# Kernel optimization log

Hardware: AMD Instinct MI355X
Metric: run time of the kernel (lower is better)

Reference implementation:

```python
import jax, jax.numpy as jnp
from jax import lax
import numpy as np

B, S, E, H, T = 32, 512, 300, 512, 9


def setup_inputs() -> dict:
    key = jax.random.key(0)
    ks = jax.random.split(key, 20)
    sc = 0.1
    inp = {
        'word_embedding': jax.random.normal(ks[0], (B, S, E), jnp.float32),
        'target_tag': jax.random.randint(ks[1], (B, S), 0, T, jnp.int64),
        'attention_masks': jnp.ones((B, S), jnp.int32),
        # layer 0 LSTM params, stacked over 2 directions; PyTorch gate order i,f,g,o
        'w_ih_l0': jax.random.normal(ks[2], (2, 4 * H, E), jnp.float32) * sc,
        'w_hh_l0': jax.random.normal(ks[3], (2, 4 * H, H), jnp.float32) * sc,
        'b_ih_l0': jax.random.normal(ks[4], (2, 4 * H), jnp.float32) * sc,
        'b_hh_l0': jax.random.normal(ks[5], (2, 4 * H), jnp.float32) * sc,
        # layer 1 takes the concatenated bidirectional output (2H)
        'w_ih_l1': jax.random.normal(ks[6], (2, 4 * H, 2 * H), jnp.float32) * sc,
        'w_hh_l1': jax.random.normal(ks[7], (2, 4 * H, H), jnp.float32) * sc,
        'b_ih_l1': jax.random.normal(ks[8], (2, 4 * H), jnp.float32) * sc,
        'b_hh_l1': jax.random.normal(ks[9], (2, 4 * H), jnp.float32) * sc,
        # hidden2tag linear
        'proj_w': jax.random.normal(ks[10], (T, 2 * H), jnp.float32) * sc,
        'proj_b': jax.random.normal(ks[11], (T,), jnp.float32) * sc,
        # CRF params
        'transitions': jax.random.normal(ks[12], (T, T), jnp.float32) * sc,
        'start_trans': jax.random.normal(ks[13], (T,), jnp.float32) * sc,
        'end_trans': jax.random.normal(ks[14], (T,), jnp.float32) * sc,
    }
    return inp


def _lstm_dir(x, w_ih, w_hh, b_ih, b_hh, reverse):
    # x: [B,S,D]; precompute input contribution for all steps, scan over time.
    h0 = jnp.zeros((x.shape[0], w_hh.shape[1]), x.dtype)
    xg = jnp.einsum('bsd,gd->sbg', x, w_ih) + b_ih  # [S,B,4H]
    if reverse:
        xg = xg[::-1]

    def step(carry, g):
        h, c = carry
        g = g + h @ w_hh.T + b_hh
        i, f, gg, o = jnp.split(g, 4, axis=-1)
        c = jax.nn.sigmoid(f) * c + jax.nn.sigmoid(i) * jnp.tanh(gg)
        h = jax.nn.sigmoid(o) * jnp.tanh(c)
        return (h, c), h

    _, hs = lax.scan(step, (h0, h0), xg)  # [S,B,H]
    if reverse:
        hs = hs[::-1]
    return jnp.swapaxes(hs, 0, 1)  # [B,S,H]


def _bilstm_layer(x, w_ih, w_hh, b_ih, b_hh):
    fwd = _lstm_dir(x, w_ih[0], w_hh[0], b_ih[0], b_hh[0], False)
    bwd = _lstm_dir(x, w_ih[1], w_hh[1], b_ih[1], b_hh[1], True)
    return jnp.concatenate([fwd, bwd], axis=-1)  # [B,S,2H]


def _crf_nll(emissions, tags, mask, trans, start, end):
    # emissions: [B,S,T]; tags: [B,S] int; mask: [B,S] bool-like (first step on)
    maskf = mask.astype(emissions.dtype)
    tags = tags.astype(jnp.int32)
    # numerator: score of the gold path
    emit_sc = jnp.take_along_axis(emissions, tags[..., None], axis=-1)[..., 0]  # [B,S]
    trans_sc = trans[tags[:, :-1], tags[:, 1:]]  # [B,S-1]
    num = start[tags[:, 0]] + emit_sc[:, 0]
    num = num + jnp.sum((emit_sc[:, 1:] + trans_sc) * maskf[:, 1:], axis=1)
    last_idx = jnp.sum(mask.astype(jnp.int32), axis=1) - 1  # [B]
    last_tag = jnp.take_along_axis(tags, last_idx[:, None], axis=1)[:, 0]
    num = num + end[last_tag]
    # denominator: forward algorithm (DP scan over time)
    alpha0 = start[None, :] + emissions[:, 0]  # [B,T]

    def step(alpha, xs):
        emit_t, m_t = xs  # [B,T], [B]
        nxt = jax.scipy.special.logsumexp(alpha[:, :, None] + trans[None], axis=1) + emit_t
        return jnp.where(m_t[:, None], nxt, alpha), None

    em_t = jnp.swapaxes(emissions, 0, 1)[1:]            # [S-1,B,T]
    m_t = jnp.swapaxes(mask, 0, 1)[1:].astype(bool)     # [S-1,B]
    alpha, _ = lax.scan(step, alpha0, (em_t, m_t))
    denom = jax.scipy.special.logsumexp(alpha + end[None, :], axis=1)  # [B]
    return -jnp.mean(num - denom)


def reference(word_embedding, target_tag, attention_masks,
              w_ih_l0, w_hh_l0, b_ih_l0, b_hh_l0,
              w_ih_l1, w_hh_l1, b_ih_l1, b_hh_l1,
              proj_w, proj_b, transitions, start_trans, end_trans):
    h = _bilstm_layer(word_embedding, w_ih_l0, w_hh_l0, b_ih_l0, b_hh_l0)
    h = _bilstm_layer(h, w_ih_l1, w_hh_l1, b_ih_l1, b_hh_l1)
    # dropout is identity in eval-mode reference
    emissions = jnp.einsum('bsh,th->bst', h, proj_w) + proj_b  # [B,S,T]
    return _crf_nll(emissions, target_tag, attention_masks,
                    transitions, start_trans, end_trans)
```

## Files before the change

### kernel.cpp

```cpp
#include <hip/hip_runtime.h>
#include <hip/hip_bf16.h>
#include <math.h>

#define S_LEN 512
#define BATCH 32
#define HDIM  512
#define NTAG  9
#define M_ROWS (S_LEN * BATCH)
#define GATES  4096

typedef __hip_bfloat16 bf16;
typedef unsigned long long ull;
typedef float f32x4 __attribute__((ext_vector_type(4)));
typedef float f32x16 __attribute__((ext_vector_type(16)));
typedef short bfrag8 __attribute__((ext_vector_type(8)));

__device__ __forceinline__ float bf2f(short s) {
    unsigned u = ((unsigned)(unsigned short)s) << 16;
    return __builtin_bit_cast(float, u);
}
__device__ __forceinline__ short f2bf(float f) {
    __hip_bfloat16 h = __float2bfloat16(f);
    return __builtin_bit_cast(short, h);
}
__device__ __forceinline__ float fsig(float x) {
    return __builtin_amdgcn_rcpf(1.f + __expf(-x));
}
__device__ __forceinline__ float ftanh(float x) {
    return 1.f - 2.f * __builtin_amdgcn_rcpf(1.f + __expf(2.f * x));
}

template <int AMODE>
__global__ __launch_bounds__(256) void gemm_xg(const void* __restrict__ Ap,
                                               const float* __restrict__ Bw,
                                               int K, int KT,
                                               const float* __restrict__ bias1,
                                               const float* __restrict__ bias2,
                                               short* __restrict__ xg) {
    __shared__ char smem[32768];
    char* As = smem;
    char* Bs = smem + 16384;
    const int tid = threadIdx.x;
    const int bm = blockIdx.y * 128;
    const int bn = blockIdx.x * 128;
    const int l  = tid & 63;
    const int wv = tid >> 6;
    const int wr = wv >> 1, wc = wv & 1;

    f32x4 acc[4][4] = {};

    const int r_st  = tid >> 1;
    const int kh    = tid & 1;
    const int xorr  = (r_st & 7) << 4;

    for (int kt = 0; kt < KT; kt++) {
        const int k0 = kt * 64;
        if (AMODE == 0) {
            const float* A = (const float*)Ap;
            int mg = bm + r_st;
            const float* arow = A + ((size_t)(mg & 31) * S_LEN + (mg >> 5)) * 300;
#pragma unroll
            for (int u = 0; u < 8; u++) {
                int kk = k0 + kh * 32 + u * 4;
                float4 v = make_float4(0.f, 0.f, 0.f, 0.f);
                if (kk + 4 <= K) v = *(const float4*)(arow + kk);
                short4 sv = make_short4(f2bf(v.x), f2bf(v.y), f2bf(v.z), f2bf(v.w));
                *(short4*)(As + ((r_st * 128 + (kh * 64 + u * 8)) ^ xorr)) = sv;
            }
        } else {
            const short* A = (const short*)Ap;
            const short* arow = A + (size_t)(bm + r_st) * 1024;
#pragma unroll
            for (int u = 0; u < 4; u++) {
                int kk = k0 + kh * 32 + u * 8;
                bfrag8 v = *(const bfrag8*)(arow + kk);
                *(bfrag8*)(As + ((r_st * 128 + (kh * 64 + u * 16)) ^ xorr)) = v;
            }
        }
        {
            const float* brow = Bw + (size_t)(bn + r_st) * K;
#pragma unroll
            for (int u = 0; u < 8; u++) {
                int kk = k0 + kh * 32 + u * 4;
                float4 v = make_float4(0.f, 0.f, 0.f, 0.f);
                if (kk + 4 <= K) v = *(const float4*)(brow + kk);
                short4 sv = make_short4(f2bf(v.x), f2bf(v.y), f2bf(v.z), f2bf(v.w));
                *(short4*)(Bs + ((r_st * 128 + (kh * 64 + u * 8)) ^ xorr)) = sv;
            }
        }
        __syncthreads();
#pragma unroll
        for (int kf = 0; kf < 2; kf++) {
            bfrag8 af[4], bfr[4];
#pragma unroll
            for (int ms = 0; ms < 4; ms++) {
                int row = wr * 64 + ms * 16 + (l & 15);
                af[ms] = *(const bfrag8*)(As + ((row * 128 + kf * 64 + (l >> 4) * 16) ^ ((row & 7) << 4)));
            }
#pragma unroll
            for (int ns = 0; ns < 4; ns++) {
                int row = wc * 64 + ns * 16 + (l & 15);
                bfr[ns] = *(const bfrag8*)(Bs + ((row * 128 + kf * 64 + (l >> 4) * 16) ^ ((row & 7) << 4)));
            }
#pragma unroll
            for (int ms = 0; ms < 4; ms++)
#pragma unroll
                for (int ns = 0; ns < 4; ns++)
                    acc[ms][ns] = __builtin_amdgcn_mfma_f32_16x16x32_bf16(af[ms], bfr[ns], acc[ms][ns], 0, 0, 0);
        }
        __syncthreads();
    }
#pragma unroll
    for (int ns = 0; ns < 4; ns++) {
        int n = bn + wc * 64 + ns * 16 + (l & 15);
        float bsum = bias1[n] + bias2[n];
#pragma unroll
        for (int ms = 0; ms < 4; ms++) {
#pragma unroll
            for (int r = 0; r < 4; r++) {
                int m = bm + wr * 64 + ms * 16 + (l >> 4) * 4 + r;
                xg[(size_t)m * GATES + n] = f2bf(acc[ms][ns][r] + bsum);
            }
        }
    }
}

__global__ __launch_bounds__(512, 1) void lstm_scan(const short* __restrict__ xg,
                                                    const float* __restrict__ whh,
                                                    ull* __restrict__ pub,
                                                    short* __restrict__ hseq) {
    const int wg  = blockIdx.x;
    const int dir = wg >> 3;
    const int p   = wg & 7;
    const int tid = threadIdx.x;
    const int wv  = tid >> 6;
    const int l   = tid & 63;
    const int g   = wv >> 1;
    const int jb  = (wv & 1) * 32;
    const int qh  = l >> 5;
    const int col = l & 31;

    __shared__ char hst[32768];
    __shared__ float Cb[4][32][64];

    bfrag8 wf[32];
    {
        const int n_row = g * 512 + p * 64 + jb + col;
        const float* sp = whh + ((size_t)dir * 2048 + n_row) * 512;
#pragma unroll
        for (int ks = 0; ks < 32; ks++) {
            const float* q = sp + ks * 16 + qh * 8;
            bfrag8 v;
#pragma unroll
            for (int u = 0; u < 8; u++) v[u] = f2bf(q[u]);
            wf[ks] = v;
        }
    }

    const int bg = tid >> 4;
    const int jq = tid & 15;
    float c4[4] = {0.f, 0.f, 0.f, 0.f};

    short4 xr_cur[4], xr_nxt[4];
    {
        const int s0 = dir ? (S_LEN - 1) : 0;
        size_t xoff = ((size_t)s0 * BATCH + bg) * GATES + dir * 2048 + p * 64 + jq * 4;
#pragma unroll
        for (int g2 = 0; g2 < 4; g2++) xr_cur[g2] = *(const short4*)(xg + xoff + g2 * 512);
    }

    for (int t = 0; t < S_LEN; t++) {
        const int s = dir ? (S_LEN - 1 - t) : t;
        {
            const int tn = (t + 1 < S_LEN) ? t + 1 : t;
            const int sn = dir ? (S_LEN - 1 - tn) : tn;
            size_t xoff = ((size_t)sn * BATCH + bg) * GATES + dir * 2048 + p * 64 + jq * 4;
#pragma unroll
            for (int g2 = 0; g2 < 4; g2++) xr_nxt[g2] = *(const short4*)(xg + xoff + g2 * 512);
        }
        const ull* src = pub + (size_t)((t & 1) * 2 + dir) * 8192;
        const unsigned expect = (unsigned)t;
        ull wvv[16];
        {
            int rounds = 0;
            bool ok;
            do {
                if (rounds++) __builtin_amdgcn_s_sleep(1);
                ok = true;
#pragma unroll
                for (int i = 0; i < 16; i++) {
                    wvv[i] = __hip_atomic_load(src + tid + i * 512, __ATOMIC_RELAXED,
                                               __HIP_MEMORY_SCOPE_AGENT);
                    ok &= ((unsigned)(wvv[i] >> 32) == expect);
                }
                if (rounds > (1 << 14)) break;
            } while (!__all(ok));
        }
#pragma unroll
        for (int i = 0; i < 16; i++) {
            int w = tid + i * 512;
            int b = w >> 8, kp = w & 255;
            *(unsigned*)(hst + ((b * 1024 + kp * 4) ^ ((b & 15) << 4))) = (unsigned)wvv[i];
        }
        __syncthreads();
        f32x16 acc = {};
#pragma unroll
        for (int ks = 0; ks < 32; ks++) {
            int byte = col * 1024 + ks * 32 + qh * 16;
            const bfrag8 a = *(const bfrag8*)(hst + (byte ^ ((col & 15) << 4)));
            acc = __builtin_amdgcn_mfma_f32_32x32x16_bf16(a, wf[ks], acc, 0, 0, 0);
        }
#pragma unroll
        for (int r = 0; r < 16; r++) {
            int brow = (r & 3) + 8 * (r >> 2) + 4 * qh;
            Cb[g][brow][jb + col] = acc[r];
        }
        __syncthreads();
        float hv[4];
        {
            float xi[4] = {bf2f(xr_cur[0].x), bf2f(xr_cur[0].y), bf2f(xr_cur[0].z), bf2f(xr_cur[0].w)};
            float xf[4] = {bf2f(xr_cur[1].x), bf2f(xr_cur[1].y), bf2f(xr_cur[1].z), bf2f(xr_cur[1].w)};
            float xc[4] = {bf2f(xr_cur[2].x), bf2f(xr_cur[2].y), bf2f(xr_cur[2].z), bf2f(xr_cur[2].w)};
            float xo[4] = {bf2f(xr_cur[3].x), bf2f(xr_cur[3].y), bf2f(xr_cur[3].z), bf2f(xr_cur[3].w)};
#pragma unroll
            for (int q = 0; q < 4; q++) {
                int jl = jq * 4 + q;
                float gi = Cb[0][bg][jl] + xi[q];
                float gf = Cb[1][bg][jl] + xf[q];
                float gc = Cb[2][bg][jl] + xc[q];
                float go = Cb[3][bg][jl] + xo[q];
                float cc = fsig(gf) * c4[q] + fsig(gi) * ftanh(gc);
                c4[q] = cc;
                hv[q] = fsig(go) * ftanh(cc);
            }
        }
        {
            unsigned short h0 = (unsigned short)f2bf(hv[0]);
            unsigned short h1 = (unsigned short)f2bf(hv[1]);
            unsigned short h2 = (unsigned short)f2bf(hv[2]);
            unsigned short h3 = (unsigned short)f2bf(hv[3]);
            ull tagw = (ull)(unsigned)(t + 1) << 32;
            ull w0 = tagw | (ull)h0 | ((ull)h1 << 16);
            ull w1 = tagw | (ull)h2 | ((ull)h3 << 16);
            ull* dst = pub + (size_t)(((t + 1) & 1) * 2 + dir) * 8192 + bg * 256 + p * 32 + jq * 2;
            __hip_atomic_store(dst, w0, __ATOMIC_RELAXED, __HIP_MEMORY_SCOPE_AGENT);
            __hip_atomic_store(dst + 1, w1, __ATOMIC_RELAXED, __HIP_MEMORY_SCOPE_AGENT);
            ull pk = (ull)h0 | ((ull)h1 << 16) | ((ull)h2 << 32) | ((ull)h3 << 48);
            ull* hd = (ull*)(hseq + ((size_t)s * BATCH + bg) * 1024 + dir * HDIM + p * 64 + jq * 4);
            __builtin_nontemporal_store(pk, hd);
        }
#pragma unroll
        for (int g2 = 0; g2 < 4; g2++) xr_cur[g2] = xr_nxt[g2];
    }
}

__global__ __launch_bounds__(256) void proj_kernel(const bf16* __restrict__ h1,
                                                   const float* __restrict__ pw,
                                                   const float* __restrict__ pb,
                                                   float* __restrict__ em) {
    __shared__ float wl[NTAG * 1024];
    __shared__ float bl[NTAG];
    for (int i = threadIdx.x; i < NTAG * 1024; i += 256) wl[i] = pw[i];
    if (threadIdx.x < NTAG) bl[threadIdx.x] = pb[threadIdx.x];
    __syncthreads();
    int m = blockIdx.x * 256 + threadIdx.x;
    int s = m >> 5, b = m & 31;
    const bf16* hr = h1 + (size_t)m * 1024;
    float acc[NTAG] = {};
    for (int k = 0; k < 1024; k += 8) {
        uint4 raw = *(const uint4*)(hr + k);
        const bf16* hv = (const bf16*)&raw;
        float hf[8];
#pragma unroll
        for (int u = 0; u < 8; u++) hf[u] = __bfloat162float(hv[u]);
#pragma unroll
        for (int tt = 0; tt < NTAG; tt++) {
            const float* wrow = &wl[tt * 1024 + k];
#pragma unroll
            for (int u = 0; u < 8; u++) acc[tt] += hf[u] * wrow[u];
        }
    }
#pragma unroll
    for (int tt = 0; tt < NTAG; tt++)
        em[((size_t)b * S_LEN + s) * NTAG + tt] = acc[tt] + bl[tt];
}

__global__ __launch_bounds__(64) void crf_kernel(const float* __restrict__ em,
                                                 const int* __restrict__ tags,
                                                 const int* __restrict__ mask,
                                                 const float* __restrict__ trans,
                                                 const float* __restrict__ startv,
                                                 const float* __restrict__ endv,
                                                 float* __restrict__ out_b) {
    int b = blockIdx.x;
    int lane = threadIdx.x;
    const float* E = em + (size_t)b * S_LEN * NTAG;
    const int* tg = tags + (size_t)b * S_LEN;
    const int* mk = mask + (size_t)b * S_LEN;

    float np = 0.f;
    int msum = 0;
    for (int s = lane; s < S_LEN; s += 64) {
        msum += (mk[s] != 0);
        if (s >= 1) {
            float mf = (float)mk[s];
            int ts = tg[s], tp = tg[s - 1];
            np += (E[(size_t)s * NTAG + ts] + trans[tp * NTAG + ts]) * mf;
        }
    }
    for (int off = 32; off; off >>= 1) {
        np += __shfl_down(np, off);
        msum += __shfl_down(msum, off);
    }
    np = __shfl(np, 0);
    msum = __shfl(msum, 0);

    int j = lane;
    float tcol[NTAG];
    if (j < NTAG)
#pragma unroll
        for (int i = 0; i < NTAG; i++) tcol[i] = trans[i * NTAG + j];
    float alpha = (j < NTAG) ? (startv[j] + E[j]) : -1e30f;
    for (int s = 1; s < S_LEN; s++) {
        float av[NTAG];
#pragma unroll
        for (int i = 0; i < NTAG; i++) av[i] = __shfl(alpha, i);
        if (j < NTAG) {
            float m = -1e30f;
#pragma unroll
            for (int i = 0; i < NTAG; i++) m = fmaxf(m, av[i] + tcol[i]);
            float ss = 0.f;
#pragma unroll
            for (int i = 0; i < NTAG; i++) ss += __expf(av[i] + tcol[i] - m);
            float nxt = m + __logf(ss) + E[(size_t)s * NTAG + j];
            if (mk[s] != 0) alpha = nxt;
        }
    }
    float val = (j < NTAG) ? (alpha + endv[j]) : -1e30f;
    float m2 = -1e30f, vv;
#pragma unroll
    for (int i = 0; i < NTAG; i++) { vv = __shfl(val, i); m2 = fmaxf(m2, vv); }
    float s2 = 0.f;
#pragma unroll
    for (int i = 0; i < NTAG; i++) { vv = __shfl(val, i); s2 += __expf(vv - m2); }
    float denom = m2 + __logf(s2);
    if (lane == 0) {
        int t0 = tg[0];
        int last = msum - 1;
        if (last < 0) last = 0;
        int lt = tg[last];
        float num = startv[t0] + E[t0] + np + endv[lt];
        out_b[b] = num - denom;
    }
}

__global__ __launch_bounds__(64) void finalize(const float* __restrict__ out_b,
                                               float* __restrict__ out) {
    int lane = threadIdx.x;
    float v = (lane < BATCH) ? out_b[lane] : 0.f;
    for (int off = 32; off; off >>= 1) v += __shfl_down(v, off);
    if (lane == 0) out[0] = -v / (float)BATCH;
}

extern "C" void kernel_launch(void* const* d_in, const int* in_sizes, int n_in,
                              void* d_out, int out_size, void* d_ws, size_t ws_size,
                              hipStream_t stream) {
    const float* x      = (const float*)d_in[0];
    const int*   tags   = (const int*)d_in[1];
    const int*   mask   = (const int*)d_in[2];
    const float* w_ih0  = (const float*)d_in[3];
    const float* w_hh0  = (const float*)d_in[4];
    const float* b_ih0  = (const float*)d_in[5];
    const float* b_hh0  = (const float*)d_in[6];
    const float* w_ih1  = (const float*)d_in[7];
    const float* w_hh1  = (const float*)d_in[8];
    const float* b_ih1  = (const float*)d_in[9];
    const float* b_hh1  = (const float*)d_in[10];
    const float* pw     = (const float*)d_in[11];
    const float* pb     = (const float*)d_in[12];
    const float* trans  = (const float*)d_in[13];
    const float* startv = (const float*)d_in[14];
    const float* endv   = (const float*)d_in[15];

    char* ws = (char*)d_ws;
    size_t off = 0;
    short* xg    = (short*)(ws + off); off += (size_t)M_ROWS * GATES * 2;
    short* hseq  = (short*)(ws + off); off += (size_t)M_ROWS * 1024 * 2;
    ull*   pub   = (ull*)(ws + off);   off += (size_t)2 * 2 * 8192 * 8;
    float* emis  = (float*)(ws + off); off += (size_t)BATCH * S_LEN * NTAG * 4;
    float* outb  = (float*)(ws + off); off += 256;
    if (off > ws_size) return;

    const size_t pub_bytes = (size_t)2 * 2 * 8192 * 8;

    gemm_xg<0><<<dim3(32, 128), 256, 0, stream>>>(x, w_ih0, 300, 5, b_ih0, b_hh0, xg);
    hipMemsetAsync(pub, 0, pub_bytes, stream);
    lstm_scan<<<16, 512, 0, stream>>>(xg, w_hh0, pub, hseq);

    gemm_xg<1><<<dim3(32, 128), 256, 0, stream>>>(hseq, w_ih1, 1024, 16, b_ih1, b_hh1, xg);
    hipMemsetAsync(pub, 0, pub_bytes, stream);
    lstm_scan<<<16, 512, 0, stream>>>(xg, w_hh1, pub, hseq);

    proj_kernel<<<M_ROWS / 256, 256, 0, stream>>>((const bf16*)hseq, pw, pb, emis);
    crf_kernel<<<BATCH, 64, 0, stream>>>(emis, tags, mask, trans, startv, endv, outb);
    finalize<<<1, 64, 0, stream>>>(outb, (float*)d_out);
}
```

Before: 6.590 ms.

## Split recurrent matmul over K halves per wave, reusing each A fragment twice

Each wave in the LSTM scan now covers one gate and half of the K dimension across both 32-column halves, instead of one gate/column half over the full K. Each LDS A-fragment load now feeds two independent MFMA chains, which halves LDS reads of h per wave and gives two interleaved accumulators for better MFMA latency hiding. The cost is a split-K partial-sum reduction through a doubled, padded Cb shared buffer, plus extra LDS traffic in the gate epilogue.

```diff
diff --git a/kernel.cpp b/kernel.cpp
--- a/kernel.cpp
+++ b/kernel.cpp
@@ -135,25 +135,26 @@
     const int tid = threadIdx.x;
     const int wv  = tid >> 6;
     const int l   = tid & 63;
-    const int g   = wv >> 1;
-    const int jb  = (wv & 1) * 32;
+    const int g   = wv & 3;
+    const int kh2 = wv >> 2;
     const int qh  = l >> 5;
     const int col = l & 31;
 
     __shared__ char hst[32768];
-    __shared__ float Cb[4][32][64];
-
-    bfrag8 wf[32];
-    {
-        const int n_row = g * 512 + p * 64 + jb + col;
-        const float* sp = whh + ((size_t)dir * 2048 + n_row) * 512;
-#pragma unroll
-        for (int ks = 0; ks < 32; ks++) {
+    __shared__ float Cb[2][4][32][65];
+
+    bfrag8 wf[2][16];
+#pragma unroll
+    for (int jj2 = 0; jj2 < 2; jj2++) {
+        const float* sp = whh + ((size_t)dir * 2048 + g * 512 + p * 64 + jj2 * 32 + col) * 512
+                        + kh2 * 256;
+#pragma unroll
+        for (int ks = 0; ks < 16; ks++) {
             const float* q = sp + ks * 16 + qh * 8;
             bfrag8 v;
 #pragma unroll
             for (int u = 0; u < 8; u++) v[u] = f2bf(q[u]);
-            wf[ks] = v;
+            wf[jj2][ks] = v;
         }
     }
 
@@ -203,17 +204,19 @@
             *(unsigned*)(hst + ((b * 1024 + kp * 4) ^ ((b & 15) << 4))) = (unsigned)wvv[i];
         }
         __syncthreads();
-        f32x16 acc = {};
-#pragma unroll
-        for (int ks = 0; ks < 32; ks++) {
-            int byte = col * 1024 + ks * 32 + qh * 16;
+        f32x16 acc0 = {}, acc1 = {};
+#pragma unroll
+        for (int ks = 0; ks < 16; ks++) {
+            int byte = col * 1024 + kh2 * 512 + ks * 32 + qh * 16;
             const bfrag8 a = *(const bfrag8*)(hst + (byte ^ ((col & 15) << 4)));
-            acc = __builtin_amdgcn_mfma_f32_32x32x16_bf16(a, wf[ks], acc, 0, 0, 0);
+            acc0 = __builtin_amdgcn_mfma_f32_32x32x16_bf16(a, wf[0][ks], acc0, 0, 0, 0);
+            acc1 = __builtin_amdgcn_mfma_f32_32x32x16_bf16(a, wf[1][ks], acc1, 0, 0, 0);
         }
 #pragma unroll
         for (int r = 0; r < 16; r++) {
             int brow = (r & 3) + 8 * (r >> 2) + 4 * qh;
-            Cb[g][brow][jb + col] = acc[r];
+            Cb[kh2][g][brow][col]      = acc0[r];
+            Cb[kh2][g][brow][32 + col] = acc1[r];
         }
         __syncthreads();
         float hv[4];
@@ -225,10 +228,10 @@
 #pragma unroll
             for (int q = 0; q < 4; q++) {
                 int jl = jq * 4 + q;
-                float gi = Cb[0][bg][jl] + xi[q];
-                float gf = Cb[1][bg][jl] + xf[q];
-                float gc = Cb[2][bg][jl] + xc[q];
-                float go = Cb[3][bg][jl] + xo[q];
+                float gi = Cb[0][0][bg][jl] + Cb[1][0][bg][jl] + xi[q];
+                float gf = Cb[0][1][bg][jl] + Cb[1][1][bg][jl] + xf[q];
+                float gc = Cb[0][2][bg][jl] + Cb[1][2][bg][jl] + xc[q];
+                float go = Cb[0][3][bg][jl] + Cb[1][3][bg][jl] + xo[q];
                 float cc = fsig(gf) * c4[q] + fsig(gi) * ftanh(gc);
                 c4[q] = cc;
                 hv[q] = fsig(go) * ftanh(cc);
```

Result: no change. 6.712 ms (+1.9%).

## Co-locate each LSTM direction's workgroups on one XCC for faster handoff

Applied to the files above, without the earlier changes.

The recurrent scan kernel now launches 256 workgroups. Each reads its hardware XCC ID and claims one of 8 roles per XCC through an atomic ticket, so both directions' 8 cooperating workgroups run on XCC 0 and XCC 1 and the rest exit right away. Keeping each direction's communicating workgroups on one XCC is meant to keep the per-step hidden-state exchange inside that XCC's shared L2 rather than crossing the die. Polling now uses volatile loads and stores, falling back to atomic loads after many rounds. A per-layer tag base plus each block seeding its own slot replaces the memset of the exchange buffer. The scheme relies on the dispatcher placing at least 8 resident blocks on each of those XCCs, and on volatile accesses giving enough visibility, otherwise the spin loop can stall until its bailout.

```diff
diff --git a/kernel.cpp b/kernel.cpp
--- a/kernel.cpp
+++ b/kernel.cpp
@@ -127,12 +127,31 @@
 
 __global__ __launch_bounds__(512, 1) void lstm_scan(const short* __restrict__ xg,
                                                     const float* __restrict__ whh,
-                                                    ull* __restrict__ pub,
-                                                    short* __restrict__ hseq) {
-    const int wg  = blockIdx.x;
-    const int dir = wg >> 3;
-    const int p   = wg & 7;
+                                                    ull* pub,
+                                                    short* __restrict__ hseq,
+                                                    int* tick,
+                                                    int tagbase) {
     const int tid = threadIdx.x;
+
+    __shared__ int role_sh;
+    if (tid == 0) {
+        unsigned xcc;
+        asm volatile("s_getreg_b32 %0, hwreg(HW_REG_XCC_ID)" : "=s"(xcc));
+        xcc &= 7;
+        int r = -1;
+        if (xcc < 2) {
+            int tk = __hip_atomic_fetch_add(&tick[xcc], 1, __ATOMIC_RELAXED,
+                                            __HIP_MEMORY_SCOPE_AGENT);
+            if (tk < 8) r = (int)xcc * 8 + tk;
+        }
+        role_sh = r;
+    }
+    __syncthreads();
+    const int role = role_sh;
+    if (role < 0) return;
+
+    const int dir = role >> 3;
+    const int p   = role & 7;
     const int wv  = tid >> 6;
     const int l   = tid & 63;
     const int g   = wv >> 1;
@@ -143,6 +162,16 @@
     __shared__ char hst[32768];
     __shared__ float Cb[4][32][64];
 
+    const int bg = tid >> 4;
+    const int jq = tid & 15;
+
+    {
+        ull tagw = (ull)(unsigned)tagbase << 32;
+        volatile ull* dst = pub + (size_t)(0 * 2 + dir) * 8192 + bg * 256 + p * 32 + jq * 2;
+        dst[0] = tagw;
+        dst[1] = tagw;
+    }
+
     bfrag8 wf[32];
     {
         const int n_row = g * 512 + p * 64 + jb + col;
@@ -157,8 +186,6 @@
         }
     }
 
-    const int bg = tid >> 4;
-    const int jq = tid & 15;
     float c4[4] = {0.f, 0.f, 0.f, 0.f};
 
     short4 xr_cur[4], xr_nxt[4];
@@ -179,22 +206,28 @@
             for (int g2 = 0; g2 < 4; g2++) xr_nxt[g2] = *(const short4*)(xg + xoff + g2 * 512);
         }
         const ull* src = pub + (size_t)((t & 1) * 2 + dir) * 8192;
-        const unsigned expect = (unsigned)t;
+        const volatile ull* srcv = (const volatile ull*)src;
+        const unsigned expect = (unsigned)(tagbase + t);
         ull wvv[16];
         {
             int rounds = 0;
-            bool ok;
-            do {
-                if (rounds++) __builtin_amdgcn_s_sleep(1);
-                ok = true;
-#pragma unroll
-                for (int i = 0; i < 16; i++) {
-                    wvv[i] = __hip_atomic_load(src + tid + i * 512, __ATOMIC_RELAXED,
-                                               __HIP_MEMORY_SCOPE_AGENT);
-                    ok &= ((unsigned)(wvv[i] >> 32) == expect);
+            for (;;) {
+                bool ok = true;
+                if (rounds < 1024) {
+#pragma unroll
+                    for (int i = 0; i < 16; i++) wvv[i] = srcv[tid + i * 512];
+                } else {
+#pragma unroll
+                    for (int i = 0; i < 16; i++)
+                        wvv[i] = __hip_atomic_load(src + tid + i * 512, __ATOMIC_RELAXED,
+                                                   __HIP_MEMORY_SCOPE_AGENT);
                 }
-                if (rounds > (1 << 14)) break;
-            } while (!__all(ok));
+#pragma unroll
+                for (int i = 0; i < 16; i++) ok &= ((unsigned)(wvv[i] >> 32) == expect);
+                if (__all(ok)) break;
+                if (++rounds > (1 << 15)) break;
+                __builtin_amdgcn_s_sleep(1);
+            }
         }
 #pragma unroll
         for (int i = 0; i < 16; i++) {
@@ -239,12 +272,12 @@
             unsigned short h1 = (unsigned short)f2bf(hv[1]);
             unsigned short h2 = (unsigned short)f2bf(hv[2]);
             unsigned short h3 = (unsigned short)f2bf(hv[3]);
-            ull tagw = (ull)(unsigned)(t + 1) << 32;
+            ull tagw = (ull)(unsigned)(tagbase + t + 1) << 32;
             ull w0 = tagw | (ull)h0 | ((ull)h1 << 16);
             ull w1 = tagw | (ull)h2 | ((ull)h3 << 16);
-            ull* dst = pub + (size_t)(((t + 1) & 1) * 2 + dir) * 8192 + bg * 256 + p * 32 + jq * 2;
-            __hip_atomic_store(dst, w0, __ATOMIC_RELAXED, __HIP_MEMORY_SCOPE_AGENT);
-            __hip_atomic_store(dst + 1, w1, __ATOMIC_RELAXED, __HIP_MEMORY_SCOPE_AGENT);
+            volatile ull* dst = pub + (size_t)(((t + 1) & 1) * 2 + dir) * 8192 + bg * 256 + p * 32 + jq * 2;
+            dst[0] = w0;
+            dst[1] = w1;
             ull pk = (ull)h0 | ((ull)h1 << 16) | ((ull)h2 << 32) | ((ull)h3 << 48);
             ull* hd = (ull*)(hseq + ((size_t)s * BATCH + bg) * 1024 + dir * HDIM + p * 64 + jq * 4);
             __builtin_nontemporal_store(pk, hd);
@@ -387,19 +420,18 @@
     short* xg    = (short*)(ws + off); off += (size_t)M_ROWS * GATES * 2;
     short* hseq  = (short*)(ws + off); off += (size_t)M_ROWS * 1024 * 2;
     ull*   pub   = (ull*)(ws + off);   off += (size_t)2 * 2 * 8192 * 8;
+    int*   tick  = (int*)(ws + off);   off += 256;
     float* emis  = (float*)(ws + off); off += (size_t)BATCH * S_LEN * NTAG * 4;
     float* outb  = (float*)(ws + off); off += 256;
     if (off > ws_size) return;
 
-    const size_t pub_bytes = (size_t)2 * 2 * 8192 * 8;
-
     gemm_xg<0><<<dim3(32, 128), 256, 0, stream>>>(x, w_ih0, 300, 5, b_ih0, b_hh0, xg);
-    hipMemsetAsync(pub, 0, pub_bytes, stream);
-    lstm_scan<<<16, 512, 0, stream>>>(xg, w_hh0, pub, hseq);
+    hipMemsetAsync(tick, 0, 256, stream);
+    lstm_scan<<<256, 512, 0, stream>>>(xg, w_hh0, pub, hseq, tick, 600);
 
     gemm_xg<1><<<dim3(32, 128), 256, 0, stream>>>(hseq, w_ih1, 1024, 16, b_ih1, b_hh1, xg);
-    hipMemsetAsync(pub, 0, pub_bytes, stream);
-    lstm_scan<<<16, 512, 0, stream>>>(xg, w_hh1, pub, hseq);
+    hipMemsetAsync(tick, 0, 256, stream);
+    lstm_scan<<<256, 512, 0, stream>>>(xg, w_hh1, pub, hseq, tick, 1200);
 
     proj_kernel<<<M_ROWS / 256, 256, 0, stream>>>((const bf16*)hseq, pw, pb, emis);
     crf_kernel<<<BATCH, 64, 0, stream>>>(emis, tags, mask, trans, startv, endv, outb);
```

Result: slower. 9.163 ms (+39.1%).
